# Kernel optimization log

Measured on AMD Instinct MI355X. Metric: run time of the kernel, lower is better.

Reference implementation:

```python
import jax, jax.numpy as jnp
import numpy as np


def _edge_softmax_by_src(e, src, n_nodes):
    # DGL edge_softmax(norm_by='src'): softmax over outgoing edges of each src node
    m = jax.ops.segment_max(e, src, num_segments=n_nodes)
    ex = jnp.exp(e - m[src])
    s = jax.ops.segment_sum(ex, src, num_segments=n_nodes)
    return ex / s[src]


def _l2norm(x):
    # F.normalize(p=2, dim=-1), eps=1e-12
    n = jnp.linalg.norm(x, axis=-1, keepdims=True)
    return x / jnp.maximum(n, 1e-12)


def setup_inputs() -> dict:
    key = jax.random.key(0)
    ks = jax.random.split(key, 16)
    N, E, D, NC = 50000, 1600000, 64, 16   # main graph nodes/edges, dim, classes
    NCL, ECL, FCL = 32, 1024, 16           # coarsened line graph: nodes=etypes
    s = 0.1
    inp = {
        "cl_h": jax.random.normal(ks[0], (NCL, FCL), jnp.float32),
        "cl_w": jax.random.normal(ks[1], (ECL,), jnp.float32),
        "cl_src": jax.random.randint(ks[2], (ECL,), 0, NCL, jnp.int32),
        "cl_dst": jax.random.randint(ks[3], (ECL,), 0, NCL, jnp.int32),
        "g_src": jax.random.randint(ks[4], (E,), 0, N, jnp.int32),
        "g_dst": jax.random.randint(ks[5], (E,), 0, N, jnp.int32),
        "g_etype": jax.random.randint(ks[6], (E,), 0, NCL, jnp.int32),
        # learned parameters
        "feats_emb": jax.random.normal(ks[7], (N, D), jnp.float32) * s,
        "W_e": jax.random.normal(ks[8], (FCL, D), jnp.float32) * s,      # linear_e (no bias)
        "beta1": jnp.array(1.0, jnp.float32),
        "eps1": jnp.array(0.0, jnp.float32),
        "beta2": jnp.array(1.0, jnp.float32),
        "eps2": jnp.array(0.0, jnp.float32),
        "W1a": jax.random.normal(ks[9], (D, D), jnp.float32) * s,
        "W2a": jax.random.normal(ks[10], (D, D), jnp.float32) * s,
        "W1b": jax.random.normal(ks[11], (D, D), jnp.float32) * s,
        "W2b": jax.random.normal(ks[12], (D, D), jnp.float32) * s,
        "W_pred": jax.random.normal(ks[13], (D, NC), jnp.float32) * s,
        "b_pred": jnp.zeros((NC,), jnp.float32),
    }
    return inp


def reference(cl_h, cl_w, cl_src, cl_dst, g_src, g_dst, g_etype,
              feats_emb, W_e, beta1, eps1, beta2, eps2,
              W1a, W2a, W1b, W2b, W_pred, b_pred):
    NCL = cl_h.shape[0]
    N = feats_emb.shape[0]

    def agnn(feat, beta, eps):
        p = _edge_softmax_by_src(beta * cl_w, cl_src, NCL)           # [Ecl]
        nh = _l2norm(feat)                                           # [NCL, F]
        agg = jax.ops.segment_sum(nh[cl_src] * p[:, None], cl_dst,
                                  num_segments=NCL)                  # [NCL, F]
        return (1.0 + eps) * feat + agg

    # edge-type feature propagation on coarsened line graph (dropout is eval-mode identity)
    h = jax.nn.relu(agnn(cl_h, beta1, eps1))
    h = jax.nn.relu(agnn(h, beta2, eps2))

    # per-edge relation embedding on main graph
    ew = h[g_etype] @ W_e                                            # [E, D]

    def gconv(feat, W1, W2):
        msg = feat[g_src] - ew                                       # u_sub_e, [E, D]
        agg = jax.ops.segment_sum(msg, g_dst, num_segments=N)        # [N, D]
        return jnp.tanh(feat @ W1 + agg @ W2)

    x = gconv(feats_emb, W1a, W2a)
    x = gconv(x, W1b, W2b)
    return x @ W_pred + b_pred
```

## Files before the change

### kernel.cpp

```cpp
#include <hip/hip_runtime.h>


#define TILE 8192

typedef __attribute__((ext_vector_type(8))) unsigned short us8;

__device__ __forceinline__ float b2f(unsigned short h) {
    return __uint_as_float(((unsigned)h) << 16);
}
__device__ __forceinline__ unsigned short f2b(float f) {
    const unsigned u = __float_as_uint(f);
    return (unsigned short)((u + 0x7FFFu + ((u >> 16) & 1u)) >> 16);
}

__device__ __forceinline__ unsigned ford_enc(float v) {
    unsigned b = __float_as_uint(v);
    return (b & 0x80000000u) ? ~b : (b | 0x80000000u);
}
__device__ __forceinline__ float ford_dec(unsigned k) {
    return __uint_as_float((k & 0x80000000u) ? (k ^ 0x80000000u) : ~k);
}

__global__ __launch_bounds__(512) void agnn_kernel(
    const float* __restrict__ cl_h, const float* __restrict__ cl_w,
    const int* __restrict__ cl_src, const int* __restrict__ cl_dst,
    const float* __restrict__ W_e,
    const float* __restrict__ pb1, const float* __restrict__ pe1,
    const float* __restrict__ pb2, const float* __restrict__ pe2,
    float* __restrict__ hW, int ECL)
{
    __shared__ float w_s[1024];
    __shared__ int   src_s[1024];
    __shared__ int   dst_s[1024];
    __shared__ float h[32][16];
    __shared__ float nh[32][16];
    __shared__ float p[1024];
    __shared__ float red[32][16];
    __shared__ float acc16[32][16][16];
    __shared__ unsigned mI[32];
    __shared__ float m[32], ssum[32], nrm[32];
    const int tid = threadIdx.x;
    const int seg = tid >> 4, j = tid & 15;

    for (int e = tid; e < ECL; e += 512) {
        w_s[e] = cl_w[e]; src_s[e] = cl_src[e]; dst_s[e] = cl_dst[e];
    }
    h[tid >> 4][tid & 15] = cl_h[tid];
    __syncthreads();

    for (int layer = 0; layer < 2; ++layer) {
        const float beta = layer ? *pb2 : *pb1;
        const float eps  = layer ? *pe2 : *pe1;

        if (tid < 32) mI[tid] = ford_enc(-3.4e38f);
        __syncthreads();
        for (int e = tid; e < ECL; e += 512)
            atomicMax(&mI[src_s[e]], ford_enc(beta * w_s[e]));
        __syncthreads();
        if (tid < 32) m[tid] = ford_dec(mI[tid]);
        __syncthreads();

        for (int e = tid; e < ECL; e += 512)
            p[e] = __expf(beta * w_s[e] - m[src_s[e]]);
        __syncthreads();

        {
            float s = 0.f;
            #pragma unroll 4
            for (int e = j; e < ECL; e += 16)
                s += (src_s[e] == seg) ? p[e] : 0.f;
            red[seg][j] = s;
        }
        __syncthreads();
        if (tid < 32) {
            float s = 0.f;
            #pragma unroll
            for (int k = 0; k < 16; ++k) s += red[tid][k];
            ssum[tid] = s;
            float q = 0.f;
            #pragma unroll
            for (int f = 0; f < 16; ++f) { float v = h[tid][f]; q += v * v; }
            nrm[tid] = fmaxf(sqrtf(q), 1e-12f);
        }
        __syncthreads();
        for (int e = tid; e < ECL; e += 512)
            p[e] = p[e] / ssum[src_s[e]];
        nh[tid >> 4][tid & 15] = h[tid >> 4][tid & 15] / nrm[tid >> 4];
        __syncthreads();

        {
            float facc[16];
            #pragma unroll
            for (int f = 0; f < 16; ++f) facc[f] = 0.f;
            #pragma unroll 4
            for (int e = j; e < ECL; e += 16) {
                if (dst_s[e] == seg) {
                    const float pe = p[e];
                    const float4* nhrow = reinterpret_cast<const float4*>(&nh[src_s[e]][0]);
                    const float4 a0 = nhrow[0], a1 = nhrow[1], a2 = nhrow[2], a3 = nhrow[3];
                    facc[0] += pe * a0.x; facc[1] += pe * a0.y; facc[2] += pe * a0.z; facc[3] += pe * a0.w;
                    facc[4] += pe * a1.x; facc[5] += pe * a1.y; facc[6] += pe * a1.z; facc[7] += pe * a1.w;
                    facc[8] += pe * a2.x; facc[9] += pe * a2.y; facc[10] += pe * a2.z; facc[11] += pe * a2.w;
                    facc[12] += pe * a3.x; facc[13] += pe * a3.y; facc[14] += pe * a3.z; facc[15] += pe * a3.w;
                }
            }
            #pragma unroll
            for (int f = 0; f < 16; ++f) acc16[seg][j][f] = facc[f];
        }
        __syncthreads();
        {
            const int t = tid >> 4, f = tid & 15;
            float a = 0.f;
            #pragma unroll
            for (int k = 0; k < 16; ++k) a += acc16[t][k][f];
            float v = (1.f + eps) * h[t][f] + a;
            h[t][f] = fmaxf(v, 0.f);
        }
        __syncthreads();
    }

    for (int o = tid; o < 2048; o += 512) {
        const int t = o >> 6, d = o & 63;
        float s = 0.f;
        #pragma unroll
        for (int f = 0; f < 16; ++f) s += h[t][f] * W_e[f * 64 + d];
        hW[o] = s;
    }
}

__global__ __launch_bounds__(256) void tobf16_kernel(
    const float* __restrict__ x, unsigned short* __restrict__ y, int total8)
{
    const int i = blockIdx.x * 256 + threadIdx.x;
    if (i >= total8) return;
    const int base = i * 8;
    const float4 a = *reinterpret_cast<const float4*>(&x[base]);
    const float4 b = *reinterpret_cast<const float4*>(&x[base + 4]);
    us8 o;
    o[0] = f2b(a.x); o[1] = f2b(a.y); o[2] = f2b(a.z); o[3] = f2b(a.w);
    o[4] = f2b(b.x); o[5] = f2b(b.y); o[6] = f2b(b.z); o[7] = f2b(b.w);
    *reinterpret_cast<us8*>(&y[base]) = o;
}

__global__ __launch_bounds__(256) void bucket_count(
    const int* __restrict__ dst, int* __restrict__ bcnt, int E)
{
    __shared__ int lh[256];
    const int tid = threadIdx.x;
    lh[tid] = 0;
    __syncthreads();
    const int base = blockIdx.x * TILE;
    #pragma unroll
    for (int it = 0; it < 8; ++it) {
        const int i = base + (it * 256 + tid) * 4;
        if (i + 3 < E) {
            const int4 d = *reinterpret_cast<const int4*>(&dst[i]);
            atomicAdd(&lh[d.x >> 8], 1); atomicAdd(&lh[d.y >> 8], 1);
            atomicAdd(&lh[d.z >> 8], 1); atomicAdd(&lh[d.w >> 8], 1);
        } else {
            for (int k = i; k < E && k < i + 4; ++k) atomicAdd(&lh[dst[k] >> 8], 1);
        }
    }
    __syncthreads();
    if (lh[tid]) atomicAdd(&bcnt[tid], lh[tid]);
}

__global__ __launch_bounds__(256) void bucket_scan(
    const int* __restrict__ bcnt, int* __restrict__ bbase, int* __restrict__ bcur)
{
    __shared__ int ws[4];
    const int tid = threadIdx.x, lane = tid & 63, wv = tid >> 6;
    const int v = bcnt[tid];
    int x = v;
    #pragma unroll
    for (int s = 1; s < 64; s <<= 1) { const int t = __shfl_up(x, s, 64); if (lane >= s) x += t; }
    if (lane == 63) ws[wv] = x;
    __syncthreads();
    if (tid == 0) { int a = ws[0]; ws[0] = 0; for (int k = 1; k < 4; ++k) { const int b = ws[k]; ws[k] = a; a += b; } }
    __syncthreads();
    const int excl = ws[wv] + x - v;
    bbase[tid] = excl; bcur[tid] = excl;
    if (tid == 255) bbase[256] = excl + v;
}

__global__ __launch_bounds__(256) void bucket_scatter(
    const int* __restrict__ src, const int* __restrict__ dst, const int* __restrict__ et,
    int* __restrict__ bcur, unsigned* __restrict__ etmp, int E)
{
    __shared__ int lh[256], lofs[256], lcur[256], gbase[256];
    __shared__ int ws[4];
    __shared__ unsigned stage[TILE];
    __shared__ unsigned char sbk[TILE];
    const int tid = threadIdx.x, lane = tid & 63, wv = tid >> 6;
    lh[tid] = 0;
    __syncthreads();
    const int base = blockIdx.x * TILE;
    #pragma unroll
    for (int it = 0; it < 8; ++it) {
        const int i = base + (it * 256 + tid) * 4;
        if (i + 3 < E) {
            const int4 d = *reinterpret_cast<const int4*>(&dst[i]);
            atomicAdd(&lh[d.x >> 8], 1); atomicAdd(&lh[d.y >> 8], 1);
            atomicAdd(&lh[d.z >> 8], 1); atomicAdd(&lh[d.w >> 8], 1);
        } else {
            for (int k = i; k < E && k < i + 4; ++k) atomicAdd(&lh[dst[k] >> 8], 1);
        }
    }
    __syncthreads();
    {
        const int v = lh[tid];
        int x = v;
        #pragma unroll
        for (int s = 1; s < 64; s <<= 1) { const int t = __shfl_up(x, s, 64); if (lane >= s) x += t; }
        if (lane == 63) ws[wv] = x;
        __syncthreads();
        if (tid == 0) { int a = ws[0]; ws[0] = 0; for (int k = 1; k < 4; ++k) { const int b = ws[k]; ws[k] = a; a += b; } }
        __syncthreads();
        const int excl = ws[wv] + x - v;
        lofs[tid] = excl; lcur[tid] = excl;
        if (v) gbase[tid] = atomicAdd(&bcur[tid], v);
    }
    __syncthreads();
    #pragma unroll
    for (int it = 0; it < 8; ++it) {
        const int i = base + (it * 256 + tid) * 4;
        if (i + 3 < E) {
            const int4 d  = *reinterpret_cast<const int4*>(&dst[i]);
            const int4 s4 = *reinterpret_cast<const int4*>(&src[i]);
            const int4 t4 = *reinterpret_cast<const int4*>(&et[i]);
            int b, r;
            b = d.x >> 8; r = atomicAdd(&lcur[b], 1);
            stage[r] = (unsigned)s4.x | ((unsigned)(d.x & 255) << 16) | ((unsigned)t4.x << 24); sbk[r] = (unsigned char)b;
            b = d.y >> 8; r = atomicAdd(&lcur[b], 1);
            stage[r] = (unsigned)s4.y | ((unsigned)(d.y & 255) << 16) | ((unsigned)t4.y << 24); sbk[r] = (unsigned char)b;
            b = d.z >> 8; r = atomicAdd(&lcur[b], 1);
            stage[r] = (unsigned)s4.z | ((unsigned)(d.z & 255) << 16) | ((unsigned)t4.z << 24); sbk[r] = (unsigned char)b;
            b = d.w >> 8; r = atomicAdd(&lcur[b], 1);
            stage[r] = (unsigned)s4.w | ((unsigned)(d.w & 255) << 16) | ((unsigned)t4.w << 24); sbk[r] = (unsigned char)b;
        } else {
            for (int k = i; k < E && k < i + 4; ++k) {
                const int b = dst[k] >> 8;
                const int r = atomicAdd(&lcur[b], 1);
                stage[r] = (unsigned)src[k] | ((unsigned)(dst[k] & 255) << 16) | ((unsigned)et[k] << 24);
                sbk[r] = (unsigned char)b;
            }
        }
    }
    __syncthreads();
    const int tot = lofs[255] + lh[255];
    for (int i = tid; i < tot; i += 256) {
        const int b = sbk[i];
        etmp[gbase[b] + (i - lofs[b])] = stage[i];
    }
}

__global__ __launch_bounds__(256) void csr_kernel(
    const unsigned* __restrict__ etmp, const int* __restrict__ bbase,
    int* __restrict__ off, unsigned* __restrict__ ssrc, int N, int NB)
{
    __shared__ int lh[256], lofs[256], lcur[256];
    __shared__ int ws[4];
    const int tid = threadIdx.x, lane = tid & 63, wv = tid >> 6;
    const int b = blockIdx.x;
    const int s = bbase[b], e = bbase[b + 1];
    lh[tid] = 0;
    __syncthreads();
    for (int i = s + tid; i < e; i += 256)
        atomicAdd(&lh[(etmp[i] >> 16) & 255], 1);
    __syncthreads();
    {
        const int v = lh[tid];
        int x = v;
        #pragma unroll
        for (int ss = 1; ss < 64; ss <<= 1) { const int t = __shfl_up(x, ss, 64); if (lane >= ss) x += t; }
        if (lane == 63) ws[wv] = x;
        __syncthreads();
        if (tid == 0) { int a = ws[0]; ws[0] = 0; for (int k = 1; k < 4; ++k) { const int c = ws[k]; ws[k] = a; a += c; } }
        __syncthreads();
        const int excl = ws[wv] + x - v;
        lofs[tid] = excl; lcur[tid] = excl;
    }
    __syncthreads();
    const int n0 = b << 8;
    if (n0 + tid < N) off[n0 + tid] = s + lofs[tid];
    if (b == NB - 1 && tid == 0) off[N] = e;
    for (int i = s + tid; i < e; i += 256) {
        const unsigned pp = etmp[i];
        const int dl = (pp >> 16) & 255;
        const int r = atomicAdd(&lcur[dl], 1);
        ssrc[s + r] = pp;
    }
}

__global__ __launch_bounds__(256) void spmm_kernel(
    const unsigned short* __restrict__ fb, const float* __restrict__ hW,
    const int* __restrict__ off, const unsigned* __restrict__ ssrc,
    float* __restrict__ aggF, int N)
{
    __shared__ float hWl[2048];
    for (int i = threadIdx.x; i < 2048; i += 256) hWl[i] = hW[i];
    __syncthreads();
    const int lane = threadIdx.x & 63;
    const int n = blockIdx.x * 4 + (threadIdx.x >> 6);
    if (n >= N) return;
    const int half = lane >> 5, c = lane & 31;
    const int beg = off[n], end = off[n + 1];
    float a0 = 0.f, a1 = 0.f;
    int i = beg + half;
    for (; i + 6 < end; i += 8) {
        unsigned pp[4];
        #pragma unroll
        for (int jj = 0; jj < 4; ++jj) pp[jj] = ssrc[i + 2 * jj];
        #pragma unroll
        for (int jj = 0; jj < 4; ++jj) {
            const unsigned u = *reinterpret_cast<const unsigned*>(
                &fb[(size_t)(pp[jj] & 0xFFFFu) * 64 + 2 * c]);
            a0 += b2f((unsigned short)(u & 0xFFFFu));
            a1 += b2f((unsigned short)(u >> 16));
        }
        #pragma unroll
        for (int jj = 0; jj < 4; ++jj) {
            const float2 hw = *reinterpret_cast<const float2*>(
                &hWl[(pp[jj] >> 24) * 64 + 2 * c]);
            a0 -= hw.x; a1 -= hw.y;
        }
    }
    for (; i < end; i += 2) {
        const unsigned pp = ssrc[i];
        const unsigned u = *reinterpret_cast<const unsigned*>(
            &fb[(size_t)(pp & 0xFFFFu) * 64 + 2 * c]);
        const float2 hw = *reinterpret_cast<const float2*>(
            &hWl[(pp >> 24) * 64 + 2 * c]);
        a0 += b2f((unsigned short)(u & 0xFFFFu)) - hw.x;
        a1 += b2f((unsigned short)(u >> 16)) - hw.y;
    }
    a0 += __shfl_xor(a0, 32);
    a1 += __shfl_xor(a1, 32);
    if (half == 0)
        *reinterpret_cast<float2*>(&aggF[(size_t)n * 64 + 2 * c]) = make_float2(a0, a1);
}

__global__ __launch_bounds__(256) void gconv_kernel(
    const float* __restrict__ Xf, const float* __restrict__ Af,
    const float* __restrict__ W1, const float* __restrict__ W2,
    float* __restrict__ x1f, unsigned short* __restrict__ out16,
    float* __restrict__ outf, int N, int final_mode,
    const float* __restrict__ Wp, const float* __restrict__ bp)
{
    __shared__ float4 fav[64 * 32];
    __shared__ float4 Wl[128 * 16];
    const int tid = threadIdx.x;
    const int ng = tid & 15, og = tid >> 4;
    const int n0 = blockIdx.x * 64;
    const int nb = ng * 4;

    #pragma unroll
    for (int q = 0; q < 8; ++q) {
        const int idx = q * 256 + tid;
        Wl[idx] = (idx < 1024)
            ? reinterpret_cast<const float4*>(W1)[idx]
            : reinterpret_cast<const float4*>(W2)[idx - 1024];
    }
    #pragma unroll
    for (int q = 0; q < 8; ++q) {
        const int cch = q * 256 + tid;
        const int row = cch >> 5, p = cch & 31;
        const int rn = n0 + row;
        float4 v = make_float4(0.f, 0.f, 0.f, 0.f);
        if (rn < N)
            v = (p < 16) ? reinterpret_cast<const float4*>(Xf)[(size_t)rn * 16 + p]
                         : reinterpret_cast<const float4*>(Af)[(size_t)rn * 16 + (p - 16)];
        fav[row * 32 + (p ^ ((row >> 2) & 7))] = v;
    }
    __syncthreads();

    float acc[4][4];
    #pragma unroll
    for (int i = 0; i < 4; ++i)
        #pragma unroll
        for (int j = 0; j < 4; ++j) acc[i][j] = 0.f;

    const int swz = ng & 7;
    #pragma unroll 2
    for (int kc = 0; kc < 32; ++kc) {
        const int pc = kc ^ swz;
        const float4 a0 = fav[(nb + 0) * 32 + pc];
        const float4 a1 = fav[(nb + 1) * 32 + pc];
        const float4 a2 = fav[(nb + 2) * 32 + pc];
        const float4 a3 = fav[(nb + 3) * 32 + pc];
        const float4 w0 = Wl[(kc * 4 + 0) * 16 + og];
        const float4 w1 = Wl[(kc * 4 + 1) * 16 + og];
        const float4 w2 = Wl[(kc * 4 + 2) * 16 + og];
        const float4 w3 = Wl[(kc * 4 + 3) * 16 + og];
        #pragma unroll
        for (int i = 0; i < 4; ++i) {
            const float4 a = (i == 0) ? a0 : (i == 1) ? a1 : (i == 2) ? a2 : a3;
            acc[i][0] += a.x * w0.x + a.y * w1.x + a.z * w2.x + a.w * w3.x;
            acc[i][1] += a.x * w0.y + a.y * w1.y + a.z * w2.y + a.w * w3.y;
            acc[i][2] += a.x * w0.z + a.y * w1.z + a.z * w2.z + a.w * w3.z;
            acc[i][3] += a.x * w0.w + a.y * w1.w + a.z * w2.w + a.w * w3.w;
        }
    }

    #pragma unroll
    for (int i = 0; i < 4; ++i)
        #pragma unroll
        for (int j = 0; j < 4; ++j) {
            const float e2 = __expf(2.f * acc[i][j]);
            acc[i][j] = 1.f - 2.f / (e2 + 1.f);
        }

    if (!final_mode) {
        #pragma unroll
        for (int i = 0; i < 4; ++i) {
            const int node = n0 + nb + i;
            if (node < N) {
                *reinterpret_cast<float4*>(&x1f[(size_t)node * 64 + og * 4]) =
                    make_float4(acc[i][0], acc[i][1], acc[i][2], acc[i][3]);
                const unsigned long long pk =
                    (unsigned long long)f2b(acc[i][0]) |
                    ((unsigned long long)f2b(acc[i][1]) << 16) |
                    ((unsigned long long)f2b(acc[i][2]) << 32) |
                    ((unsigned long long)f2b(acc[i][3]) << 48);
                *reinterpret_cast<unsigned long long*>(&out16[(size_t)node * 64 + og * 4]) = pk;
            }
        }
    } else {
        float* TL = reinterpret_cast<float*>(fav);
        __syncthreads();
        #pragma unroll
        for (int i = 0; i < 4; ++i)
            #pragma unroll
            for (int j = 0; j < 4; ++j)
                TL[(nb + i) * 65 + og * 4 + j] = acc[i][j];
        __syncthreads();
        const int l = tid & 63, cg = (tid >> 6) * 4;
        float o0 = bp[cg], o1 = bp[cg + 1], o2 = bp[cg + 2], o3 = bp[cg + 3];
        for (int d = 0; d < 64; ++d) {
            const float tv = TL[l * 65 + d];
            const float4 wp = *reinterpret_cast<const float4*>(&Wp[d * 16 + cg]);
            o0 += tv * wp.x; o1 += tv * wp.y; o2 += tv * wp.z; o3 += tv * wp.w;
        }
        const int node = n0 + l;
        if (node < N)
            *reinterpret_cast<float4*>(&outf[(size_t)node * 16 + cg]) =
                make_float4(o0, o1, o2, o3);
    }
}

extern "C" void kernel_launch(void* const* d_in, const int* in_sizes, int n_in,
                              void* d_out, int out_size, void* d_ws, size_t ws_size,
                              hipStream_t stream)
{
    const float* cl_h   = (const float*)d_in[0];
    const float* cl_w   = (const float*)d_in[1];
    const int*   cl_src = (const int*)d_in[2];
    const int*   cl_dst = (const int*)d_in[3];
    const int*   g_src  = (const int*)d_in[4];
    const int*   g_dst  = (const int*)d_in[5];
    const int*   g_et   = (const int*)d_in[6];
    const float* feats  = (const float*)d_in[7];
    const float* W_e    = (const float*)d_in[8];
    const float* b1     = (const float*)d_in[9];
    const float* e1     = (const float*)d_in[10];
    const float* b2     = (const float*)d_in[11];
    const float* e2     = (const float*)d_in[12];
    const float* W1a    = (const float*)d_in[13];
    const float* W2a    = (const float*)d_in[14];
    const float* W1b    = (const float*)d_in[15];
    const float* W2b    = (const float*)d_in[16];
    const float* Wp     = (const float*)d_in[17];
    const float* bp     = (const float*)d_in[18];
    const int ECL = in_sizes[1];
    const int E   = in_sizes[4];
    const int N   = in_sizes[7] / 64;
    const int NB  = (N + 255) >> 8;

    char* w = (char*)d_ws;
    auto carve = [&](size_t bytes) {
        char* r = w;
        w += (bytes + 255) & ~(size_t)255;
        return r;
    };
    float*          hW    = (float*)carve(32 * 64 * sizeof(float));
    int*            off   = (int*)carve((size_t)(N + 1) * sizeof(int));
    int*            bcnt  = (int*)carve(256 * sizeof(int));
    int*            bbase = (int*)carve(257 * sizeof(int));
    int*            bcur  = (int*)carve(256 * sizeof(int));
    unsigned*       etmp  = (unsigned*)carve((size_t)E * sizeof(unsigned));
    unsigned*       ssrc  = (unsigned*)carve((size_t)E * sizeof(unsigned));
    unsigned short* fb16  = (unsigned short*)carve((size_t)N * 64 * sizeof(unsigned short));
    unsigned short* x16   = (unsigned short*)carve((size_t)N * 64 * sizeof(unsigned short));
    float*          aggF  = (float*)carve((size_t)N * 64 * sizeof(float));
    float*          x1f   = (float*)carve((size_t)N * 64 * sizeof(float));

    const int nblk = (E + TILE - 1) / TILE;
    const int total8 = N * 8;

    hipMemsetAsync(bcnt, 0, 256 * sizeof(int), stream);

    agnn_kernel<<<1, 512, 0, stream>>>(cl_h, cl_w, cl_src, cl_dst, W_e,
                                       b1, e1, b2, e2, hW, ECL);
    tobf16_kernel<<<(total8 + 255) / 256, 256, 0, stream>>>(feats, fb16, total8);
    bucket_count<<<nblk, 256, 0, stream>>>(g_dst, bcnt, E);
    bucket_scan<<<1, 256, 0, stream>>>(bcnt, bbase, bcur);
    bucket_scatter<<<nblk, 256, 0, stream>>>(g_src, g_dst, g_et, bcur, etmp, E);
    csr_kernel<<<NB, 256, 0, stream>>>(etmp, bbase, off, ssrc, N, NB);
    spmm_kernel<<<(N + 3) / 4, 256, 0, stream>>>(fb16, hW, off, ssrc, aggF, N);
    gconv_kernel<<<(N + 63) / 64, 256, 0, stream>>>(feats, aggF, W1a, W2a,
                                                    x1f, x16, nullptr, N, 0, Wp, bp);
    spmm_kernel<<<(N + 3) / 4, 256, 0, stream>>>(x16, hW, off, ssrc, aggF, N);
    gconv_kernel<<<(N + 63) / 64, 256, 0, stream>>>(x1f, aggF, W1b, W2b,
                                                    nullptr, nullptr, (float*)d_out, N, 1, Wp, bp);
}
```

Baseline: 235.1 us.

## Split SpMM feature columns across blocks and fold bucket-count reset into AGNN kernel

The SpMM kernel now splits the 64 feature columns into two 32-column groups handled by separate blocks. Each wave covers one node's half-row, with 4 edge slots of 16 lanes and 4 independent gathers per slot per iteration. This is meant to raise memory-level parallelism and cut per-lane serial work, at the cost of doubling the edge-index reads, issuing narrower gathers and adding a second cross-lane reduction step. Separately, the hipMemsetAsync that zeroes the bucket counters is dropped and done inside the AGNN kernel, saving one stream operation.

```diff
diff --git a/kernel.cpp b/kernel.cpp
--- a/kernel.cpp
+++ b/kernel.cpp
@@ -27,7 +27,7 @@
     const float* __restrict__ W_e,
     const float* __restrict__ pb1, const float* __restrict__ pe1,
     const float* __restrict__ pb2, const float* __restrict__ pe2,
-    float* __restrict__ hW, int ECL)
+    float* __restrict__ hW, int* __restrict__ bcnt, int ECL)
 {
     __shared__ float w_s[1024];
     __shared__ int   src_s[1024];
@@ -41,6 +41,8 @@
     __shared__ float m[32], ssum[32], nrm[32];
     const int tid = threadIdx.x;
     const int seg = tid >> 4, j = tid & 15;
+
+    if (tid < 256) bcnt[tid] = 0;
 
     for (int e = tid; e < ECL; e += 512) {
         w_s[e] = cl_w[e]; src_s[e] = cl_src[e]; dst_s[e] = cl_dst[e];
@@ -300,44 +302,48 @@
     __shared__ float hWl[2048];
     for (int i = threadIdx.x; i < 2048; i += 256) hWl[i] = hW[i];
     __syncthreads();
+    const int bid = blockIdx.x;
+    const int cg  = (bid >> 2) & 1;
+    const int ng  = (bid >> 3) * 4 + (bid & 3);
+    const int n = ng * 4 + (threadIdx.x >> 6);
+    if (n >= N) return;
     const int lane = threadIdx.x & 63;
-    const int n = blockIdx.x * 4 + (threadIdx.x >> 6);
-    if (n >= N) return;
-    const int half = lane >> 5, c = lane & 31;
+    const int slot = lane >> 4;
+    const int dbase = cg * 32 + 2 * (lane & 15);
     const int beg = off[n], end = off[n + 1];
     float a0 = 0.f, a1 = 0.f;
-    int i = beg + half;
-    for (; i + 6 < end; i += 8) {
+    int i = beg;
+    for (; i + 15 < end; i += 16) {
         unsigned pp[4];
         #pragma unroll
-        for (int jj = 0; jj < 4; ++jj) pp[jj] = ssrc[i + 2 * jj];
-        #pragma unroll
-        for (int jj = 0; jj < 4; ++jj) {
-            const unsigned u = *reinterpret_cast<const unsigned*>(
-                &fb[(size_t)(pp[jj] & 0xFFFFu) * 64 + 2 * c]);
-            a0 += b2f((unsigned short)(u & 0xFFFFu));
-            a1 += b2f((unsigned short)(u >> 16));
-        }
-        #pragma unroll
-        for (int jj = 0; jj < 4; ++jj) {
+        for (int j = 0; j < 4; ++j) pp[j] = ssrc[i + 4 * j + slot];
+        unsigned u[4];
+        #pragma unroll
+        for (int j = 0; j < 4; ++j)
+            u[j] = *reinterpret_cast<const unsigned*>(
+                &fb[(size_t)(pp[j] & 0xFFFFu) * 64 + dbase]);
+        #pragma unroll
+        for (int j = 0; j < 4; ++j) {
             const float2 hw = *reinterpret_cast<const float2*>(
-                &hWl[(pp[jj] >> 24) * 64 + 2 * c]);
-            a0 -= hw.x; a1 -= hw.y;
-        }
-    }
-    for (; i < end; i += 2) {
-        const unsigned pp = ssrc[i];
+                &hWl[(pp[j] >> 24) * 64 + dbase]);
+            a0 += b2f((unsigned short)(u[j] & 0xFFFFu)) - hw.x;
+            a1 += b2f((unsigned short)(u[j] >> 16)) - hw.y;
+        }
+    }
+    for (int e = i + slot; e < end; e += 4) {
+        const unsigned pp = ssrc[e];
         const unsigned u = *reinterpret_cast<const unsigned*>(
-            &fb[(size_t)(pp & 0xFFFFu) * 64 + 2 * c]);
+            &fb[(size_t)(pp & 0xFFFFu) * 64 + dbase]);
         const float2 hw = *reinterpret_cast<const float2*>(
-            &hWl[(pp >> 24) * 64 + 2 * c]);
+            &hWl[(pp >> 24) * 64 + dbase]);
         a0 += b2f((unsigned short)(u & 0xFFFFu)) - hw.x;
         a1 += b2f((unsigned short)(u >> 16)) - hw.y;
     }
-    a0 += __shfl_xor(a0, 32);
-    a1 += __shfl_xor(a1, 32);
-    if (half == 0)
-        *reinterpret_cast<float2*>(&aggF[(size_t)n * 64 + 2 * c]) = make_float2(a0, a1);
+    a0 += __shfl_xor(a0, 16); a0 += __shfl_xor(a0, 32);
+    a1 += __shfl_xor(a1, 16); a1 += __shfl_xor(a1, 32);
+    if (slot == 0)
+        *reinterpret_cast<float2*>(&aggF[(size_t)n * 64 + dbase]) =
+            make_float2(a0, a1);
 }
 
 __global__ __launch_bounds__(256) void gconv_kernel(
@@ -496,20 +502,20 @@
 
     const int nblk = (E + TILE - 1) / TILE;
     const int total8 = N * 8;
-
-    hipMemsetAsync(bcnt, 0, 256 * sizeof(int), stream);
+    const int nng = (N + 3) / 4;
+    const int spmm_grid = ((nng + 3) / 4) * 8;
 
     agnn_kernel<<<1, 512, 0, stream>>>(cl_h, cl_w, cl_src, cl_dst, W_e,
-                                       b1, e1, b2, e2, hW, ECL);
+                                       b1, e1, b2, e2, hW, bcnt, ECL);
     tobf16_kernel<<<(total8 + 255) / 256, 256, 0, stream>>>(feats, fb16, total8);
     bucket_count<<<nblk, 256, 0, stream>>>(g_dst, bcnt, E);
     bucket_scan<<<1, 256, 0, stream>>>(bcnt, bbase, bcur);
     bucket_scatter<<<nblk, 256, 0, stream>>>(g_src, g_dst, g_et, bcur, etmp, E);
     csr_kernel<<<NB, 256, 0, stream>>>(etmp, bbase, off, ssrc, N, NB);
-    spmm_kernel<<<(N + 3) / 4, 256, 0, stream>>>(fb16, hW, off, ssrc, aggF, N);
+    spmm_kernel<<<spmm_grid, 256, 0, stream>>>(fb16, hW, off, ssrc, aggF, N);
     gconv_kernel<<<(N + 63) / 64, 256, 0, stream>>>(feats, aggF, W1a, W2a,
                                                     x1f, x16, nullptr, N, 0, Wp, bp);
-    spmm_kernel<<<(N + 3) / 4, 256, 0, stream>>>(x16, hW, off, ssrc, aggF, N);
+    spmm_kernel<<<spmm_grid, 256, 0, stream>>>(x16, hW, off, ssrc, aggF, N);
     gconv_kernel<<<(N + 63) / 64, 256, 0, stream>>>(x1f, aggF, W1b, W2b,
                                                     nullptr, nullptr, (float*)d_out, N, 1, Wp, bp);
 }
```

New measurement: 274.6 us. 16.8% more time.
